# Kernel optimization log

Measured on AMD Instinct MI355X. Metric: run time of the kernel, lower is better.

Reference implementation:

```python
import jax, jax.numpy as jnp
import numpy as np

B, N_PER, E_PER = 100, 1000, 12000  # graphs, nodes/graph, edges/graph
N, E = B * N_PER, B * E_PER
K = int(np.ceil(0.8 * N_PER))  # TopKPooling ratio=0.8 -> 800 kept nodes/graph


def setup_inputs() -> dict:
    key = jax.random.key(0)
    ks = jax.random.split(key, 16)
    g = jnp.repeat(jnp.arange(B, dtype=jnp.int64), E_PER)
    src = g * N_PER + jax.random.randint(ks[0], (E,), 0, N_PER)
    dst = g * N_PER + jax.random.randint(ks[1], (E,), 0, N_PER)
    edge_index = jnp.stack([src, dst]).astype(jnp.int64)
    edge_attr = jax.random.uniform(ks[2], (E,), dtype=jnp.float32) + 0.1  # positive edge weights
    x = jax.random.normal(ks[3], (N, 3), dtype=jnp.float32)
    batch = jnp.repeat(jnp.arange(B, dtype=jnp.int64), N_PER)
    s = 0.1
    return {
        'x': x, 'edge_index': edge_index, 'edge_attr': edge_attr, 'batch': batch,
        'conv1_w': jax.random.normal(ks[4], (3, 64), dtype=jnp.float32) * s,
        'conv1_b': jnp.zeros((64,), dtype=jnp.float32),
        'conv2_w': jax.random.normal(ks[5], (64, 64), dtype=jnp.float32) * s,
        'conv2_b': jnp.zeros((64,), dtype=jnp.float32),
        'pool_w': jax.random.normal(ks[6], (64,), dtype=jnp.float32) * s,
        'lin1_w': jax.random.normal(ks[7], (64, 64), dtype=jnp.float32) * s,
        'lin1_b': jnp.zeros((64,), dtype=jnp.float32),
        'lin2_w': jax.random.normal(ks[8], (64, 32), dtype=jnp.float32) * s,
        'lin2_b': jnp.zeros((32,), dtype=jnp.float32),
        'lin3_w': jax.random.normal(ks[9], (32, 1), dtype=jnp.float32) * s,
        'lin3_b': jnp.zeros((1,), dtype=jnp.float32),
    }


def gcn_conv(x, row, col, ew, W, b):
    # PyG GCNConv with edge_weight and implicit self-loops (weight 1):
    # deg[i] = sum_{e: col=i} ew[e] + 1;  norm_e = d^{-1/2}[row]*ew*d^{-1/2}[col]
    h = x @ W  # [N, out]
    deg = jax.ops.segment_sum(ew, col, num_segments=N) + 1.0
    dinv = jax.lax.rsqrt(deg)
    msg = (dinv[row] * ew * dinv[col])[:, None] * h[row]  # [E, out]
    out = jax.ops.segment_sum(msg, col, num_segments=N)
    out = out + (dinv * dinv)[:, None] * h  # self-loop term
    return out + b


def reference(x, edge_index, edge_attr, batch, conv1_w, conv1_b, conv2_w, conv2_b,
              pool_w, lin1_w, lin1_b, lin2_w, lin2_b, lin3_w, lin3_b):
    row, col = edge_index[0], edge_index[1]
    h = jax.nn.relu(gcn_conv(x, row, col, edge_attr, conv1_w, conv1_b))
    x1 = h.reshape(B, N_PER, 64).mean(axis=1)  # global_mean_pool (equal-size graphs)
    h = jax.nn.relu(gcn_conv(h, row, col, edge_attr, conv2_w, conv2_b))
    # TopKPooling: score = tanh(x.w / ||w||), keep top-K per graph, gate by score
    score = jnp.tanh(h @ pool_w / jnp.linalg.norm(pool_w))  # [N]
    score_bn = score.reshape(B, N_PER)
    vals, idx = jax.lax.top_k(score_bn, K)  # [B, K]
    h_bn = h.reshape(B, N_PER, 64)
    h_sel = jnp.take_along_axis(h_bn, idx[..., None], axis=1) * vals[..., None]
    x2 = h_sel.mean(axis=1)  # global_mean_pool on pooled graph
    z = x1 + x2
    z = jax.nn.relu(z @ lin1_w + lin1_b)
    z = jax.nn.relu(z @ lin2_w + lin2_b)  # dropout is identity in eval mode
    out = jax.nn.sigmoid(z @ lin3_w + lin3_b)[:, 0]
    return out
```

## Files before the change

### kernel.cpp

```cpp
#include <hip/hip_runtime.h>

#define B_G   100
#define N_PER 1000
#define E_PER 12000
#define NTOT  (B_G * N_PER)
#define ETOT  (B_G * E_PER)
#define KSEL  800
#define EPT   12

typedef __attribute__((ext_vector_type(8))) short short8;
typedef __attribute__((ext_vector_type(4))) float float4_;

__device__ __forceinline__ unsigned short f2bf(float f) {
    unsigned u = __float_as_uint(f);
    u += 0x7fffu + ((u >> 16) & 1u);
    return (unsigned short)(u >> 16);
}
__device__ __forceinline__ float upk(unsigned q) {
    return __uint_as_float(q & 0xFFFF0000u);
}
__device__ __forceinline__ float dec_raw(unsigned byte7f) {
    return __uint_as_float(byte7f << 20);
}
__device__ __forceinline__ unsigned enc_fp8(float z) {
    unsigned u = __float_as_uint(z * 0x1p-120f);
    u += 0x7FFFFu + ((u >> 20) & 1u);
    return u >> 20;
}

#define CONV2_TI(TI, AF0, AF1) do {                                            \
    const int t_ = wid + (TI) * 16;                                            \
    const int li_ = t_ * 16 + nloc;                                            \
    const bool valid_ = li_ < N_PER;                                           \
    float acc_[16];                                                            \
    int s_ = 0, cn_ = 0;                                                       \
    if (valid_) {                                                              \
        uint4 rv_ = *(const uint4*)(zs + li_ * 64 + ((kgrp ^ ((li_ >> 1) & 3)) << 4)); \
        _Pragma("unroll")                                                      \
        for (int j = 0; j < 4; j++) {                                          \
            acc_[j]      = dec_raw((rv_.x >> (8 * j)) & 0x7Fu);                \
            acc_[4 + j]  = dec_raw((rv_.y >> (8 * j)) & 0x7Fu);                \
            acc_[8 + j]  = dec_raw((rv_.z >> (8 * j)) & 0x7Fu);                \
            acc_[12 + j] = dec_raw((rv_.w >> (8 * j)) & 0x7Fu);                \
        }                                                                      \
        s_ = li_ ? ends[li_ - 1] : 0;                                          \
        cn_ = ends[li_] - s_;                                                  \
    } else {                                                                   \
        _Pragma("unroll")                                                      \
        for (int j = 0; j < 16; j++) acc_[j] = 0.f;                            \
    }                                                                          \
    int mx_ = cn_;                                                             \
    _Pragma("unroll")                                                          \
    for (int m = 1; m < 16; m <<= 1) mx_ = max(mx_, __shfl_xor(mx_, m));       \
    for (int k = 0; k < mx_; k++) {                                            \
        if (k < cn_) {                                                         \
            unsigned q_ = csr[s_ + k];                                         \
            int src_ = (int)(q_ & 0xFFFFu);                                    \
            float wv_ = upk(q_);                                               \
            uint4 rv_ = *(const uint4*)(zs + src_ * 64 + ((kgrp ^ ((src_ >> 1) & 3)) << 4)); \
            _Pragma("unroll")                                                  \
            for (int j = 0; j < 4; j++) {                                      \
                acc_[j]      += wv_ * dec_raw((rv_.x >> (8 * j)) & 0x7Fu);     \
                acc_[4 + j]  += wv_ * dec_raw((rv_.y >> (8 * j)) & 0x7Fu);     \
                acc_[8 + j]  += wv_ * dec_raw((rv_.z >> (8 * j)) & 0x7Fu);     \
                acc_[12 + j] += wv_ * dec_raw((rv_.w >> (8 * j)) & 0x7Fu);     \
            }                                                                  \
        }                                                                      \
    }                                                                          \
    float scale_ = (valid_ ? dl[li_] : 0.f) * 0x1p120f;                        \
    _Pragma("unroll")                                                          \
    for (int j = 0; j < 8; j++) {                                              \
        AF0[j] = (short)f2bf(scale_ * acc_[j]);                                \
        AF1[j] = (short)f2bf(scale_ * acc_[8 + j]);                            \
    }                                                                          \
} while (0)

#define W2_TI(TI, AF0, AF1) do {                                               \
    const int t_ = wid + (TI) * 16;                                            \
    if (t_ < 63) {                                                             \
        float4_ accv_[4];                                                      \
        _Pragma("unroll")                                                      \
        for (int c = 0; c < 4; ++c) accv_[c] = (float4_){0.f, 0.f, 0.f, 0.f};  \
        _Pragma("unroll")                                                      \
        for (int c = 0; c < 4; ++c) {                                          \
            accv_[c] = __builtin_amdgcn_mfma_f32_16x16x32_bf16(AF0, Bf[0][c], accv_[c], 0, 0, 0); \
            accv_[c] = __builtin_amdgcn_mfma_f32_16x16x32_bf16(AF1, Bf[1][c], accv_[c], 0, 0, 0); \
        }                                                                      \
        _Pragma("unroll")                                                      \
        for (int r2 = 0; r2 < 4; ++r2) {                                       \
            int li2_ = t_ * 16 + kgrp * 4 + r2;                                \
            bool valid2_ = li2_ < N_PER;                                       \
            float sp_ = 0.f;                                                   \
            _Pragma("unroll")                                                  \
            for (int c = 0; c < 4; ++c) {                                      \
                float hv_ = fmaxf(accv_[c][r2] + b2c[c], 0.f);                 \
                sp_ += hv_ * pwc[c];                                           \
                if (valid2_) zs[li2_ * 64 + c * 16 + nloc] = (unsigned char)enc_fp8(hv_); \
            }                                                                  \
            _Pragma("unroll")                                                  \
            for (int m = 1; m < 16; m <<= 1) sp_ += __shfl_xor(sp_, m);        \
            if (valid2_ && nloc == 0) {                                        \
                float scv_ = tanhf(sp_ * invn);                                \
                unsigned bits_ = __float_as_uint(scv_);                        \
                unsigned u_ = (bits_ & 0x80000000u) ? ~bits_ : (bits_ | 0x80000000u); \
                keys[li2_] = ((unsigned long long)u_ << 32) | (unsigned)(1023 - li2_); \
            }                                                                  \
        }                                                                      \
    }                                                                          \
} while (0)

#define FRONT_BODY() do {                                                      \
    int esrc[EPT], edst[EPT]; float eww[EPT];                                  \
    int ne = (tid < (E_PER - (EPT - 1) * 1024)) ? EPT : EPT - 1;               \
    _Pragma("unroll")                                                          \
    for (int i = 0; i < EPT; i++) {                                            \
        if (i < ne) {                                                          \
            int e = tid + i * 1024;                                            \
            esrc[i] = ei[ebase + e] - gbase;                                   \
            edst[i] = ei[ETOT + ebase + e] - gbase;                            \
            eww[i]  = ew[ebase + e];                                           \
        }                                                                      \
    }                                                                          \
    ends[tid] = 0;                                                             \
    for (int i = tid; i < N_PER * 3; i += 1024) xl[i] = x[(size_t)gbase * 3 + i]; \
    __syncthreads();                                                           \
    _Pragma("unroll")                                                          \
    for (int i = 0; i < EPT; i++)                                              \
        if (i < ne) atomicAdd(&ends[edst[i]], 1);                              \
    __syncthreads();                                                           \
    int v = ends[tid];                                                         \
    int sc = v;                                                                \
    _Pragma("unroll")                                                          \
    for (int m = 1; m < 64; m <<= 1) {                                         \
        int t = __shfl_up(sc, m);                                              \
        if (lane >= m) sc += t;                                                \
    }                                                                          \
    if (lane == 63) wpart[wid] = sc;                                           \
    __syncthreads();                                                           \
    if (tid < 16) {                                                            \
        int s2 = wpart[tid];                                                   \
        _Pragma("unroll")                                                      \
        for (int m = 1; m < 16; m <<= 1) {                                     \
            int t = __shfl_up(s2, m);                                          \
            if (tid >= m) s2 += t;                                             \
        }                                                                      \
        wpart[tid] = s2;                                                       \
    }                                                                          \
    __syncthreads();                                                           \
    int incl = sc + (wid > 0 ? wpart[wid - 1] : 0);                            \
    ends[tid] = incl;                                                          \
    posc[tid] = incl - v;                                                      \
    __syncthreads();                                                           \
    _Pragma("unroll")                                                          \
    for (int i = 0; i < EPT; i++)                                              \
        if (i < ne) {                                                          \
            int p = atomicAdd(&posc[edst[i]], 1);                              \
            csr[p] = ((unsigned)f2bf(eww[i]) << 16) | (unsigned)esrc[i];       \
        }                                                                      \
    __syncthreads();                                                           \
    float dmy = 0.f;                                                           \
    int s0i = 0, e0i = 0;                                                      \
    if (tid < N_PER) {                                                         \
        s0i = tid ? ends[tid - 1] : 0;                                         \
        e0i = ends[tid];                                                       \
        float s0 = 0.f, s1 = 0.f;                                              \
        int k = s0i;                                                           \
        for (; k + 2 <= e0i; k += 2) { s0 += upk(csr[k]); s1 += upk(csr[k + 1]); } \
        if (k < e0i) s0 += upk(csr[k]);                                        \
        dmy = rsqrtf(s0 + s1 + 1.0f);                                          \
        dl[tid] = dmy;                                                         \
        xl[tid * 3 + 0] *= dmy;                                                \
        xl[tid * 3 + 1] *= dmy;                                                \
        xl[tid * 3 + 2] *= dmy;                                                \
    }                                                                          \
    __syncthreads();                                                           \
    if (tid < N_PER) {                                                         \
        float a0 = xl[tid * 3 + 0], a1 = xl[tid * 3 + 1], a2 = xl[tid * 3 + 2];\
        for (int k = s0i; k < e0i; k++) {                                      \
            unsigned q = csr[k];                                               \
            int i0 = (int)(q & 0xFFFFu) * 3;                                   \
            float wv = upk(q);                                                 \
            a0 += wv * xl[i0]; a1 += wv * xl[i0 + 1]; a2 += wv * xl[i0 + 2];   \
        }                                                                      \
        aggv[tid * 3 + 0] = dmy * a0;                                          \
        aggv[tid * 3 + 1] = dmy * a1;                                          \
        aggv[tid * 3 + 2] = dmy * a2;                                          \
    }                                                                          \
    __syncthreads();                                                           \
    {                                                                          \
        float w0 = w1[lane], w1v = w1[64 + lane], w2v = w1[128 + lane], bf = b1[lane]; \
        float* sred = (float*)(uA + 12288);                                    \
        float px = 0.f;                                                        \
        int chunk = (lane & 31) >> 3;                                          \
        int word  = ((lane >= 32) ? 2 : 0) + ((lane & 7) >> 2);                \
        for (int node = wid; node < N_PER; node += 16) {                       \
            float a0 = aggv[node * 3], a1 = aggv[node * 3 + 1], a2 = aggv[node * 3 + 2]; \
            float hv = fmaxf(a0 * w0 + a1 * w1v + a2 * w2v + bf, 0.f);         \
            px += hv;                                                          \
            unsigned byte = enc_fp8(dl[node] * hv);                            \
            unsigned t1 = __shfl_xor(byte, 1);                                 \
            unsigned v16 = (lane & 1) ? (t1 | (byte << 8)) : (byte | (t1 << 8)); \
            unsigned t2 = __shfl_xor(v16, 2);                                  \
            unsigned v32 = (lane & 2) ? (t2 | (v16 << 16)) : (v16 | (t2 << 16)); \
            if ((lane & 3) == 0) {                                             \
                int cs = chunk ^ ((node >> 1) & 3);                            \
                *(unsigned*)(zs + node * 64 + cs * 16 + word * 4) = v32;       \
            }                                                                  \
        }                                                                      \
        sred[wid * 64 + lane] = px;                                            \
        __syncthreads();                                                       \
        if (tid < 64) {                                                        \
            float t = 0.f;                                                     \
            for (int r = 0; r < 16; r++) t += sred[r * 64 + tid];              \
            x1b[tid] = t * (1.0f / N_PER);                                     \
        }                                                                      \
    }                                                                          \
} while (0)

#define W2_SETUP() do {                                                        \
    _Pragma("unroll")                                                          \
    for (int kh = 0; kh < 2; ++kh)                                             \
        _Pragma("unroll")                                                      \
        for (int c = 0; c < 4; ++c) {                                          \
            short8 t;                                                          \
            _Pragma("unroll")                                                  \
            for (int j = 0; j < 8; ++j)                                        \
                t[j] = (short)f2bf(w2[(kh * 32 + kgrp * 8 + j) * 64 + c * 16 + nloc]); \
            Bf[kh][c] = t;                                                     \
        }                                                                      \
    _Pragma("unroll")                                                          \
    for (int c = 0; c < 4; ++c) {                                              \
        b2c[c] = b2[c * 16 + nloc];                                            \
        pwc[c] = pw[c * 16 + nloc];                                            \
    }                                                                          \
    {                                                                          \
        float p = pw[lane], pn = p * p;                                        \
        _Pragma("unroll")                                                      \
        for (int m = 32; m; m >>= 1) pn += __shfl_xor(pn, m);                  \
        invn = rsqrtf(pn);                                                     \
    }                                                                          \
} while (0)

#define TAIL_BODY(OUTIDX) do {                                                 \
    {                                                                          \
        unsigned long long key = keys[tid];                                    \
        for (int k = 2; k <= 1024; k <<= 1) {                                  \
            for (int j = k >> 1; j > 0; j >>= 1) {                             \
                bool desc = (tid & k) == 0;                                    \
                unsigned long long p;                                          \
                if (j >= 64) {                                                 \
                    keys[tid] = key;                                           \
                    __syncthreads();                                           \
                    p = keys[tid ^ j];                                         \
                    __syncthreads();                                           \
                } else {                                                       \
                    p = __shfl_xor(key, j);                                    \
                }                                                              \
                bool low = (tid & j) == 0;                                     \
                bool sw = low ? (desc ? (key < p) : (key > p))                 \
                              : (desc ? (p < key) : (p > key));                \
                if (sw) key = p;                                               \
            }                                                                  \
        }                                                                      \
        keys[tid] = key;                                                       \
    }                                                                          \
    __syncthreads();                                                           \
    float* red   = (float*)(uA + 8192);                                        \
    float* a1buf = (float*)(uA + 12288);                                       \
    float* a2buf = (float*)(uA + 12544);                                       \
    float* zbuf  = (float*)(uA + 12672);                                       \
    {                                                                          \
        int f = tid & 63, w16 = tid >> 6;                                      \
        float acc2 = 0.f;                                                      \
        for (int r = w16; r < KSEL; r += 16) {                                 \
            unsigned long long key = keys[r];                                  \
            int idx = 1023 - (int)(key & 0xFFFFFFFFu);                         \
            unsigned u = (unsigned)(key >> 32);                                \
            unsigned bits = (u & 0x80000000u) ? (u & 0x7FFFFFFFu) : ~u;        \
            float valS = __uint_as_float(bits) * 0x1p120f;                     \
            acc2 += valS * dec_raw((unsigned)zs[idx * 64 + f] & 0x7Fu);        \
        }                                                                      \
        red[tid] = acc2;                                                       \
    }                                                                          \
    __syncthreads();                                                           \
    if (tid < 64) {                                                            \
        float s2 = 0.f;                                                        \
        for (int ww = 0; ww < 16; ww++) s2 += red[ww * 64 + tid];              \
        zbuf[tid] = x1b[tid] + s2 * (1.0f / KSEL);                             \
    }                                                                          \
    __syncthreads();                                                           \
    if (tid < 64) {                                                            \
        float a = l1b[tid];                                                    \
        for (int k = 0; k < 64; k++) a += zbuf[k] * l1w[k * 64 + tid];         \
        a1buf[tid] = fmaxf(a, 0.f);                                            \
    }                                                                          \
    __syncthreads();                                                           \
    if (tid < 32) {                                                            \
        float a = l2b[tid];                                                    \
        for (int k = 0; k < 64; k++) a += a1buf[k] * l2w[k * 32 + tid];        \
        a2buf[tid] = fmaxf(a, 0.f);                                            \
    }                                                                          \
    __syncthreads();                                                           \
    if (tid == 0) {                                                            \
        float t = l3b[0];                                                      \
        for (int k = 0; k < 32; k++) t += a2buf[k] * l3w[k];                   \
        out[OUTIDX] = 1.0f / (1.0f + expf(-t));                                \
    }                                                                          \
} while (0)

#define SMEM_DECLS()                                                           \
    __shared__ __align__(16) unsigned char smem[136832];                       \
    unsigned char* zs = smem;                                                  \
    float* xl = (float*)smem;                                                  \
    unsigned* csr = (unsigned*)(smem + 64000);                                 \
    int*   ends = (int*)(smem + 112000);                                       \
    float* dl   = (float*)(smem + 116096);                                     \
    int*   posc = (int*)(smem + 116096);                                       \
    int*   wpart = (int*)(smem + 120192);                                      \
    float* x1b   = (float*)(smem + 120192);                                    \
    unsigned char* uA = smem + 120448;                                         \
    float* aggv = (float*)uA;

#define PARAMS                                                                 \
    const int* __restrict__ ei, const float* __restrict__ ew,                  \
    const float* __restrict__ x,                                               \
    const float* __restrict__ w1, const float* __restrict__ b1,                \
    const float* __restrict__ w2, const float* __restrict__ b2,                \
    const float* __restrict__ pw,                                              \
    const float* __restrict__ l1w, const float* __restrict__ l1b,              \
    const float* __restrict__ l2w, const float* __restrict__ l2b,              \
    const float* __restrict__ l3w, const float* __restrict__ l3b,              \
    float* __restrict__ out

__global__ __launch_bounds__(1024)
__attribute__((amdgpu_waves_per_eu(4, 4))) void k_all_single(PARAMS) {
    SMEM_DECLS();
    int g = blockIdx.x, tid = threadIdx.x;
    int wid = tid >> 6, lane = tid & 63;
    int gbase = g * N_PER, ebase = g * E_PER;
    FRONT_BODY();
    int kgrp = lane >> 4, nloc = lane & 15;
    short8 Af0a, Af0b, Af1a, Af1b, Af2a, Af2b, Af3a, Af3b;
    CONV2_TI(0, Af0a, Af0b);
    CONV2_TI(1, Af1a, Af1b);
    CONV2_TI(2, Af2a, Af2b);
    CONV2_TI(3, Af3a, Af3b);
    __syncthreads();
    unsigned long long* keys = (unsigned long long*)uA;
    {
        short8 Bf[2][4]; float b2c[4], pwc[4], invn;
        W2_SETUP();
        if (tid >= N_PER) keys[tid] = 0ull;
        W2_TI(0, Af0a, Af0b);
        W2_TI(1, Af1a, Af1b);
        W2_TI(2, Af2a, Af2b);
        W2_TI(3, Af3a, Af3b);
    }
    __syncthreads();
    TAIL_BODY(g);
}

__global__ __launch_bounds__(1024)
__attribute__((amdgpu_waves_per_eu(4, 4))) void k_all_pair(
    PARAMS, unsigned char* __restrict__ ws) {
    SMEM_DECLS();
    int g = blockIdx.x >> 1, half = blockIdx.x & 1, tid = threadIdx.x;
    int wid = tid >> 6, lane = tid & 63;
    int gbase = g * N_PER, ebase = g * E_PER;
    unsigned int* flag = (unsigned int*)ws;
    unsigned char* h2x = ws + 4096 + (size_t)g * 32768;
    unsigned long long* kx =
        (unsigned long long*)(ws + 4096 + 100 * 32768 + (size_t)g * 4096);

    FRONT_BODY();
    int kgrp = lane >> 4, nloc = lane & 15;
    const int tiA = half * 2, tiB = half * 2 + 1;
    short8 AfAa, AfAb, AfBa, AfBb;
    CONV2_TI(tiA, AfAa, AfAb);
    CONV2_TI(tiB, AfBa, AfBb);
    __syncthreads();
    unsigned long long* keys = (unsigned long long*)uA;
    {
        short8 Bf[2][4]; float b2c[4], pwc[4], invn;
        W2_SETUP();
        if (tid >= N_PER) keys[tid] = 0ull;
        W2_TI(tiA, AfAa, AfAb);
        W2_TI(tiB, AfBa, AfBb);
    }
    __syncthreads();
    if (half) {
        const uint4* srcv = (const uint4*)(zs + 32768);
        uint4* dstv = (uint4*)h2x;
        for (int i = tid; i < 1952; i += 1024) dstv[i] = srcv[i];
        for (int i = tid; i < 512; i += 1024) kx[i] = keys[512 + i];
        __syncthreads();
        if (tid == 0)
            __hip_atomic_store(flag + g, 1u, __ATOMIC_RELEASE,
                               __HIP_MEMORY_SCOPE_AGENT);
        return;
    }
    if (tid == 0) {
        for (int it = 0; it < 1000000; ++it) {
            if (__hip_atomic_load(flag + g, __ATOMIC_ACQUIRE,
                                  __HIP_MEMORY_SCOPE_AGENT) != 0u) break;
            __builtin_amdgcn_s_sleep(8);
        }
    }
    __syncthreads();
    {
        uint4* dstv = (uint4*)(zs + 32768);
        const uint4* srcv = (const uint4*)h2x;
        for (int i = tid; i < 1952; i += 1024) dstv[i] = srcv[i];
        for (int i = tid; i < 512; i += 1024) keys[512 + i] = kx[i];
    }
    __syncthreads();
    TAIL_BODY(g);
}

extern "C" void kernel_launch(void* const* d_in, const int* in_sizes, int n_in,
                              void* d_out, int out_size, void* d_ws, size_t ws_size,
                              hipStream_t stream) {
    const float* x   = (const float*)d_in[0];
    const int*   ei  = (const int*)d_in[1];
    const float* ew  = (const float*)d_in[2];
    const float* c1w = (const float*)d_in[4];
    const float* c1b = (const float*)d_in[5];
    const float* c2w = (const float*)d_in[6];
    const float* c2b = (const float*)d_in[7];
    const float* pw  = (const float*)d_in[8];
    const float* l1w = (const float*)d_in[9];
    const float* l1b = (const float*)d_in[10];
    const float* l2w = (const float*)d_in[11];
    const float* l2b = (const float*)d_in[12];
    const float* l3w = (const float*)d_in[13];
    const float* l3b = (const float*)d_in[14];
    float* out = (float*)d_out;
    (void)in_sizes; (void)n_in; (void)out_size;

    const size_t needed = 4096 + (size_t)100 * 32768 + (size_t)100 * 4096;
    if (d_ws != nullptr && ws_size >= needed) {
        hipMemsetAsync(d_ws, 0, 512, stream);
        k_all_pair<<<2 * B_G, 1024, 0, stream>>>(
            ei, ew, x, c1w, c1b, c2w, c2b, pw,
            l1w, l1b, l2w, l2b, l3w, l3b, out, (unsigned char*)d_ws);
    } else {
        k_all_single<<<B_G, 1024, 0, stream>>>(
            ei, ew, x, c1w, c1b, c2w, c2b, pw,
            l1w, l1b, l2w, l2b, l3w, l3b, out);
    }
}
```

Baseline: 171.3 us.

## Split fused pair kernel into build, mid and tail kernels via workspace

Replaces the single 200-block kernel, where block pairs per graph synchronize through a global flag spin-wait, with three launches. The first builds the CSR per graph, the second runs conv1/conv2 split across two blocks per graph, and the third does top-k and the MLP. Each stage hands its data to the next through global workspace. This removes the intra-kernel spin wait and the duplicated CSR build across both halves, at the cost of two extra launches and extra global round-trips for the CSR, h2 and keys.

```diff
diff --git a/kernel.cpp b/kernel.cpp
--- a/kernel.cpp
+++ b/kernel.cpp
@@ -8,6 +8,13 @@
 #define KSEL  800
 #define EPT   12
 
+#define CSRB  0u
+#define ENDB  4915200u
+#define H2B   5324800u
+#define KEYB  11878400u
+#define X1BB  12697600u
+#define WSNEED 12723200u
+
 typedef __attribute__((ext_vector_type(8))) short short8;
 typedef __attribute__((ext_vector_type(4))) float float4_;
 
@@ -28,88 +35,7 @@
     return u >> 20;
 }
 
-#define CONV2_TI(TI, AF0, AF1) do {                                            \
-    const int t_ = wid + (TI) * 16;                                            \
-    const int li_ = t_ * 16 + nloc;                                            \
-    const bool valid_ = li_ < N_PER;                                           \
-    float acc_[16];                                                            \
-    int s_ = 0, cn_ = 0;                                                       \
-    if (valid_) {                                                              \
-        uint4 rv_ = *(const uint4*)(zs + li_ * 64 + ((kgrp ^ ((li_ >> 1) & 3)) << 4)); \
-        _Pragma("unroll")                                                      \
-        for (int j = 0; j < 4; j++) {                                          \
-            acc_[j]      = dec_raw((rv_.x >> (8 * j)) & 0x7Fu);                \
-            acc_[4 + j]  = dec_raw((rv_.y >> (8 * j)) & 0x7Fu);                \
-            acc_[8 + j]  = dec_raw((rv_.z >> (8 * j)) & 0x7Fu);                \
-            acc_[12 + j] = dec_raw((rv_.w >> (8 * j)) & 0x7Fu);                \
-        }                                                                      \
-        s_ = li_ ? ends[li_ - 1] : 0;                                          \
-        cn_ = ends[li_] - s_;                                                  \
-    } else {                                                                   \
-        _Pragma("unroll")                                                      \
-        for (int j = 0; j < 16; j++) acc_[j] = 0.f;                            \
-    }                                                                          \
-    int mx_ = cn_;                                                             \
-    _Pragma("unroll")                                                          \
-    for (int m = 1; m < 16; m <<= 1) mx_ = max(mx_, __shfl_xor(mx_, m));       \
-    for (int k = 0; k < mx_; k++) {                                            \
-        if (k < cn_) {                                                         \
-            unsigned q_ = csr[s_ + k];                                         \
-            int src_ = (int)(q_ & 0xFFFFu);                                    \
-            float wv_ = upk(q_);                                               \
-            uint4 rv_ = *(const uint4*)(zs + src_ * 64 + ((kgrp ^ ((src_ >> 1) & 3)) << 4)); \
-            _Pragma("unroll")                                                  \
-            for (int j = 0; j < 4; j++) {                                      \
-                acc_[j]      += wv_ * dec_raw((rv_.x >> (8 * j)) & 0x7Fu);     \
-                acc_[4 + j]  += wv_ * dec_raw((rv_.y >> (8 * j)) & 0x7Fu);     \
-                acc_[8 + j]  += wv_ * dec_raw((rv_.z >> (8 * j)) & 0x7Fu);     \
-                acc_[12 + j] += wv_ * dec_raw((rv_.w >> (8 * j)) & 0x7Fu);     \
-            }                                                                  \
-        }                                                                      \
-    }                                                                          \
-    float scale_ = (valid_ ? dl[li_] : 0.f) * 0x1p120f;                        \
-    _Pragma("unroll")                                                          \
-    for (int j = 0; j < 8; j++) {                                              \
-        AF0[j] = (short)f2bf(scale_ * acc_[j]);                                \
-        AF1[j] = (short)f2bf(scale_ * acc_[8 + j]);                            \
-    }                                                                          \
-} while (0)
-
-#define W2_TI(TI, AF0, AF1) do {                                               \
-    const int t_ = wid + (TI) * 16;                                            \
-    if (t_ < 63) {                                                             \
-        float4_ accv_[4];                                                      \
-        _Pragma("unroll")                                                      \
-        for (int c = 0; c < 4; ++c) accv_[c] = (float4_){0.f, 0.f, 0.f, 0.f};  \
-        _Pragma("unroll")                                                      \
-        for (int c = 0; c < 4; ++c) {                                          \
-            accv_[c] = __builtin_amdgcn_mfma_f32_16x16x32_bf16(AF0, Bf[0][c], accv_[c], 0, 0, 0); \
-            accv_[c] = __builtin_amdgcn_mfma_f32_16x16x32_bf16(AF1, Bf[1][c], accv_[c], 0, 0, 0); \
-        }                                                                      \
-        _Pragma("unroll")                                                      \
-        for (int r2 = 0; r2 < 4; ++r2) {                                       \
-            int li2_ = t_ * 16 + kgrp * 4 + r2;                                \
-            bool valid2_ = li2_ < N_PER;                                       \
-            float sp_ = 0.f;                                                   \
-            _Pragma("unroll")                                                  \
-            for (int c = 0; c < 4; ++c) {                                      \
-                float hv_ = fmaxf(accv_[c][r2] + b2c[c], 0.f);                 \
-                sp_ += hv_ * pwc[c];                                           \
-                if (valid2_) zs[li2_ * 64 + c * 16 + nloc] = (unsigned char)enc_fp8(hv_); \
-            }                                                                  \
-            _Pragma("unroll")                                                  \
-            for (int m = 1; m < 16; m <<= 1) sp_ += __shfl_xor(sp_, m);        \
-            if (valid2_ && nloc == 0) {                                        \
-                float scv_ = tanhf(sp_ * invn);                                \
-                unsigned bits_ = __float_as_uint(scv_);                        \
-                unsigned u_ = (bits_ & 0x80000000u) ? ~bits_ : (bits_ | 0x80000000u); \
-                keys[li2_] = ((unsigned long long)u_ << 32) | (unsigned)(1023 - li2_); \
-            }                                                                  \
-        }                                                                      \
-    }                                                                          \
-} while (0)
-
-#define FRONT_BODY() do {                                                      \
+#define BUILD_BODY(PRE) do {                                                   \
     int esrc[EPT], edst[EPT]; float eww[EPT];                                  \
     int ne = (tid < (E_PER - (EPT - 1) * 1024)) ? EPT : EPT - 1;               \
     _Pragma("unroll")                                                          \
@@ -122,7 +48,7 @@
         }                                                                      \
     }                                                                          \
     ends[tid] = 0;                                                             \
-    for (int i = tid; i < N_PER * 3; i += 1024) xl[i] = x[(size_t)gbase * 3 + i]; \
+    PRE                                                                        \
     __syncthreads();                                                           \
     _Pragma("unroll")                                                          \
     for (int i = 0; i < EPT; i++)                                              \
@@ -158,6 +84,9 @@
             csr[p] = ((unsigned)f2bf(eww[i]) << 16) | (unsigned)esrc[i];       \
         }                                                                      \
     __syncthreads();                                                           \
+} while (0)
+
+#define REST_BODY() do {                                                       \
     float dmy = 0.f;                                                           \
     int s0i = 0, e0i = 0;                                                      \
     if (tid < N_PER) {                                                         \
@@ -213,6 +142,87 @@
             float t = 0.f;                                                     \
             for (int r = 0; r < 16; r++) t += sred[r * 64 + tid];              \
             x1b[tid] = t * (1.0f / N_PER);                                     \
+        }                                                                      \
+    }                                                                          \
+} while (0)
+
+#define CONV2_TI(TI, AF0, AF1) do {                                            \
+    const int t_ = wid + (TI) * 16;                                            \
+    const int li_ = t_ * 16 + nloc;                                            \
+    const bool valid_ = li_ < N_PER;                                           \
+    float acc_[16];                                                            \
+    int s_ = 0, cn_ = 0;                                                       \
+    if (valid_) {                                                              \
+        uint4 rv_ = *(const uint4*)(zs + li_ * 64 + ((kgrp ^ ((li_ >> 1) & 3)) << 4)); \
+        _Pragma("unroll")                                                      \
+        for (int j = 0; j < 4; j++) {                                          \
+            acc_[j]      = dec_raw((rv_.x >> (8 * j)) & 0x7Fu);                \
+            acc_[4 + j]  = dec_raw((rv_.y >> (8 * j)) & 0x7Fu);                \
+            acc_[8 + j]  = dec_raw((rv_.z >> (8 * j)) & 0x7Fu);                \
+            acc_[12 + j] = dec_raw((rv_.w >> (8 * j)) & 0x7Fu);                \
+        }                                                                      \
+        s_ = li_ ? ends[li_ - 1] : 0;                                          \
+        cn_ = ends[li_] - s_;                                                  \
+    } else {                                                                   \
+        _Pragma("unroll")                                                      \
+        for (int j = 0; j < 16; j++) acc_[j] = 0.f;                            \
+    }                                                                          \
+    int mx_ = cn_;                                                             \
+    _Pragma("unroll")                                                          \
+    for (int m = 1; m < 16; m <<= 1) mx_ = max(mx_, __shfl_xor(mx_, m));       \
+    for (int k = 0; k < mx_; k++) {                                            \
+        if (k < cn_) {                                                         \
+            unsigned q_ = csr[s_ + k];                                         \
+            int src_ = (int)(q_ & 0xFFFFu);                                    \
+            float wv_ = upk(q_);                                               \
+            uint4 rv_ = *(const uint4*)(zs + src_ * 64 + ((kgrp ^ ((src_ >> 1) & 3)) << 4)); \
+            _Pragma("unroll")                                                  \
+            for (int j = 0; j < 4; j++) {                                      \
+                acc_[j]      += wv_ * dec_raw((rv_.x >> (8 * j)) & 0x7Fu);     \
+                acc_[4 + j]  += wv_ * dec_raw((rv_.y >> (8 * j)) & 0x7Fu);     \
+                acc_[8 + j]  += wv_ * dec_raw((rv_.z >> (8 * j)) & 0x7Fu);     \
+                acc_[12 + j] += wv_ * dec_raw((rv_.w >> (8 * j)) & 0x7Fu);     \
+            }                                                                  \
+        }                                                                      \
+    }                                                                          \
+    float scale_ = (valid_ ? dl[li_] : 0.f) * 0x1p120f;                        \
+    _Pragma("unroll")                                                          \
+    for (int j = 0; j < 8; j++) {                                              \
+        AF0[j] = (short)f2bf(scale_ * acc_[j]);                                \
+        AF1[j] = (short)f2bf(scale_ * acc_[8 + j]);                            \
+    }                                                                          \
+} while (0)
+
+#define W2_TI(TI, AF0, AF1) do {                                               \
+    const int t_ = wid + (TI) * 16;                                            \
+    if (t_ < 63) {                                                             \
+        float4_ accv_[4];                                                      \
+        _Pragma("unroll")                                                      \
+        for (int c = 0; c < 4; ++c) accv_[c] = (float4_){0.f, 0.f, 0.f, 0.f};  \
+        _Pragma("unroll")                                                      \
+        for (int c = 0; c < 4; ++c) {                                          \
+            accv_[c] = __builtin_amdgcn_mfma_f32_16x16x32_bf16(AF0, Bf[0][c], accv_[c], 0, 0, 0); \
+            accv_[c] = __builtin_amdgcn_mfma_f32_16x16x32_bf16(AF1, Bf[1][c], accv_[c], 0, 0, 0); \
+        }                                                                      \
+        _Pragma("unroll")                                                      \
+        for (int r2 = 0; r2 < 4; ++r2) {                                       \
+            int li2_ = t_ * 16 + kgrp * 4 + r2;                                \
+            bool valid2_ = li2_ < N_PER;                                       \
+            float sp_ = 0.f;                                                   \
+            _Pragma("unroll")                                                  \
+            for (int c = 0; c < 4; ++c) {                                      \
+                float hv_ = fmaxf(accv_[c][r2] + b2c[c], 0.f);                 \
+                sp_ += hv_ * pwc[c];                                           \
+                if (valid2_) zs[li2_ * 64 + c * 16 + nloc] = (unsigned char)enc_fp8(hv_); \
+            }                                                                  \
+            _Pragma("unroll")                                                  \
+            for (int m = 1; m < 16; m <<= 1) sp_ += __shfl_xor(sp_, m);        \
+            if (valid2_ && nloc == 0) {                                        \
+                float scv_ = tanhf(sp_ * invn);                                \
+                unsigned bits_ = __float_as_uint(scv_);                        \
+                unsigned u_ = (bits_ & 0x80000000u) ? ~bits_ : (bits_ | 0x80000000u); \
+                keys[li2_] = ((unsigned long long)u_ << 32) | (unsigned)(1023 - li2_); \
+            }                                                                  \
         }                                                                      \
     }                                                                          \
 } while (0)
@@ -265,10 +275,6 @@
         keys[tid] = key;                                                       \
     }                                                                          \
     __syncthreads();                                                           \
-    float* red   = (float*)(uA + 8192);                                        \
-    float* a1buf = (float*)(uA + 12288);                                       \
-    float* a2buf = (float*)(uA + 12544);                                       \
-    float* zbuf  = (float*)(uA + 12672);                                       \
     {                                                                          \
         int f = tid & 63, w16 = tid >> 6;                                      \
         float acc2 = 0.f;                                                      \
@@ -319,26 +325,118 @@
     int*   wpart = (int*)(smem + 120192);                                      \
     float* x1b   = (float*)(smem + 120192);                                    \
     unsigned char* uA = smem + 120448;                                         \
-    float* aggv = (float*)uA;
-
-#define PARAMS                                                                 \
-    const int* __restrict__ ei, const float* __restrict__ ew,                  \
-    const float* __restrict__ x,                                               \
-    const float* __restrict__ w1, const float* __restrict__ b1,                \
-    const float* __restrict__ w2, const float* __restrict__ b2,                \
-    const float* __restrict__ pw,                                              \
-    const float* __restrict__ l1w, const float* __restrict__ l1b,              \
-    const float* __restrict__ l2w, const float* __restrict__ l2b,              \
-    const float* __restrict__ l3w, const float* __restrict__ l3b,              \
-    float* __restrict__ out
+    float* aggv = (float*)uA;                                                  \
+    (void)posc; (void)wpart; (void)aggv;
+
+__global__ __launch_bounds__(1024) void k_build(
+    const int* __restrict__ ei, const float* __restrict__ ew,
+    unsigned char* __restrict__ ws) {
+    __shared__ __align__(16) unsigned csr[12000];
+    __shared__ int ends[1024];
+    __shared__ int posc[1024];
+    __shared__ int wpart[16];
+    int g = blockIdx.x, tid = threadIdx.x;
+    int wid = tid >> 6, lane = tid & 63;
+    int gbase = g * N_PER, ebase = g * E_PER;
+    BUILD_BODY();
+    {
+        uint4* cw = (uint4*)(ws + CSRB + (size_t)g * 49152);
+        const uint4* cs = (const uint4*)csr;
+        for (int i = tid; i < 3000; i += 1024) cw[i] = cs[i];
+        ((int*)(ws + ENDB + (size_t)g * 4096))[tid] = ends[tid];
+    }
+}
 
 __global__ __launch_bounds__(1024)
-__attribute__((amdgpu_waves_per_eu(4, 4))) void k_all_single(PARAMS) {
+__attribute__((amdgpu_waves_per_eu(4, 4))) void k_mid(
+    const float* __restrict__ x,
+    const float* __restrict__ w1, const float* __restrict__ b1,
+    const float* __restrict__ w2, const float* __restrict__ b2,
+    const float* __restrict__ pw, unsigned char* __restrict__ ws) {
+    SMEM_DECLS();
+    int g = blockIdx.x >> 1, half = blockIdx.x & 1, tid = threadIdx.x;
+    int wid = tid >> 6, lane = tid & 63;
+    int gbase = g * N_PER;
+    {
+        const uint4* cs = (const uint4*)(ws + CSRB + (size_t)g * 49152);
+        uint4* cd = (uint4*)csr;
+        for (int i = tid; i < 3000; i += 1024) cd[i] = cs[i];
+        ends[tid] = ((const int*)(ws + ENDB + (size_t)g * 4096))[tid];
+        for (int i = tid; i < N_PER * 3; i += 1024) xl[i] = x[(size_t)gbase * 3 + i];
+    }
+    __syncthreads();
+    REST_BODY();
+    int kgrp = lane >> 4, nloc = lane & 15;
+    const int tiA = half * 2, tiB = half * 2 + 1;
+    short8 AfAa, AfAb, AfBa, AfBb;
+    CONV2_TI(tiA, AfAa, AfAb);
+    CONV2_TI(tiB, AfBa, AfBb);
+    __syncthreads();
+    unsigned long long* keys = (unsigned long long*)uA;
+    {
+        short8 Bf[2][4]; float b2c[4], pwc[4], invn;
+        W2_SETUP();
+        if (tid >= N_PER) keys[tid] = 0ull;
+        W2_TI(tiA, AfAa, AfAb);
+        W2_TI(tiB, AfBa, AfBb);
+    }
+    __syncthreads();
+    {
+        uint4* d = (uint4*)(ws + H2B + (size_t)g * 65536 + (size_t)half * 32768);
+        const uint4* s = (const uint4*)(zs + half * 32768);
+        int n = half ? 1952 : 2048;
+        for (int i = tid; i < n; i += 1024) d[i] = s[i];
+        unsigned long long* kw =
+            (unsigned long long*)(ws + KEYB + (size_t)g * 8192);
+        for (int i = tid; i < 512; i += 1024)
+            kw[half * 512 + i] = keys[half * 512 + i];
+        if (!half && tid < 64)
+            ((float*)(ws + X1BB + (size_t)g * 256))[tid] = x1b[tid];
+    }
+}
+
+__global__ __launch_bounds__(1024) void k_tail(
+    const float* __restrict__ l1w, const float* __restrict__ l1b,
+    const float* __restrict__ l2w, const float* __restrict__ l2b,
+    const float* __restrict__ l3w, const float* __restrict__ l3b,
+    float* __restrict__ out, const unsigned char* __restrict__ ws) {
+    __shared__ __align__(16) unsigned char sm2[77184];
+    unsigned char* zs = sm2;
+    unsigned long long* keys = (unsigned long long*)(sm2 + 64000);
+    float* red   = (float*)(sm2 + 72192);
+    float* x1b   = (float*)(sm2 + 76288);
+    float* a1buf = (float*)(sm2 + 76544);
+    float* a2buf = (float*)(sm2 + 76800);
+    float* zbuf  = (float*)(sm2 + 76928);
+    int g = blockIdx.x, tid = threadIdx.x;
+    {
+        uint4* hd = (uint4*)zs;
+        const uint4* hs = (const uint4*)(ws + H2B + (size_t)g * 65536);
+        for (int i = tid; i < 4000; i += 1024) hd[i] = hs[i];
+        keys[tid] = ((const unsigned long long*)(ws + KEYB + (size_t)g * 8192))[tid];
+        if (tid < 64) x1b[tid] = ((const float*)(ws + X1BB + (size_t)g * 256))[tid];
+    }
+    __syncthreads();
+    TAIL_BODY(g);
+}
+
+__global__ __launch_bounds__(1024)
+__attribute__((amdgpu_waves_per_eu(4, 4))) void k_all_single(
+    const int* __restrict__ ei, const float* __restrict__ ew,
+    const float* __restrict__ x,
+    const float* __restrict__ w1, const float* __restrict__ b1,
+    const float* __restrict__ w2, const float* __restrict__ b2,
+    const float* __restrict__ pw,
+    const float* __restrict__ l1w, const float* __restrict__ l1b,
+    const float* __restrict__ l2w, const float* __restrict__ l2b,
+    const float* __restrict__ l3w, const float* __restrict__ l3b,
+    float* __restrict__ out) {
     SMEM_DECLS();
     int g = blockIdx.x, tid = threadIdx.x;
     int wid = tid >> 6, lane = tid & 63;
     int gbase = g * N_PER, ebase = g * E_PER;
-    FRONT_BODY();
+    BUILD_BODY(for (int i = tid; i < N_PER * 3; i += 1024) xl[i] = x[(size_t)gbase * 3 + i];);
+    REST_BODY();
     int kgrp = lane >> 4, nloc = lane & 15;
     short8 Af0a, Af0b, Af1a, Af1b, Af2a, Af2b, Af3a, Af3b;
     CONV2_TI(0, Af0a, Af0b);
@@ -357,63 +455,10 @@
         W2_TI(3, Af3a, Af3b);
     }
     __syncthreads();
-    TAIL_BODY(g);
-}
-
-__global__ __launch_bounds__(1024)
-__attribute__((amdgpu_waves_per_eu(4, 4))) void k_all_pair(
-    PARAMS, unsigned char* __restrict__ ws) {
-    SMEM_DECLS();
-    int g = blockIdx.x >> 1, half = blockIdx.x & 1, tid = threadIdx.x;
-    int wid = tid >> 6, lane = tid & 63;
-    int gbase = g * N_PER, ebase = g * E_PER;
-    unsigned int* flag = (unsigned int*)ws;
-    unsigned char* h2x = ws + 4096 + (size_t)g * 32768;
-    unsigned long long* kx =
-        (unsigned long long*)(ws + 4096 + 100 * 32768 + (size_t)g * 4096);
-
-    FRONT_BODY();
-    int kgrp = lane >> 4, nloc = lane & 15;
-    const int tiA = half * 2, tiB = half * 2 + 1;
-    short8 AfAa, AfAb, AfBa, AfBb;
-    CONV2_TI(tiA, AfAa, AfAb);
-    CONV2_TI(tiB, AfBa, AfBb);
-    __syncthreads();
-    unsigned long long* keys = (unsigned long long*)uA;
-    {
-        short8 Bf[2][4]; float b2c[4], pwc[4], invn;
-        W2_SETUP();
-        if (tid >= N_PER) keys[tid] = 0ull;
-        W2_TI(tiA, AfAa, AfAb);
-        W2_TI(tiB, AfBa, AfBb);
-    }
-    __syncthreads();
-    if (half) {
-        const uint4* srcv = (const uint4*)(zs + 32768);
-        uint4* dstv = (uint4*)h2x;
-        for (int i = tid; i < 1952; i += 1024) dstv[i] = srcv[i];
-        for (int i = tid; i < 512; i += 1024) kx[i] = keys[512 + i];
-        __syncthreads();
-        if (tid == 0)
-            __hip_atomic_store(flag + g, 1u, __ATOMIC_RELEASE,
-                               __HIP_MEMORY_SCOPE_AGENT);
-        return;
-    }
-    if (tid == 0) {
-        for (int it = 0; it < 1000000; ++it) {
-            if (__hip_atomic_load(flag + g, __ATOMIC_ACQUIRE,
-                                  __HIP_MEMORY_SCOPE_AGENT) != 0u) break;
-            __builtin_amdgcn_s_sleep(8);
-        }
-    }
-    __syncthreads();
-    {
-        uint4* dstv = (uint4*)(zs + 32768);
-        const uint4* srcv = (const uint4*)h2x;
-        for (int i = tid; i < 1952; i += 1024) dstv[i] = srcv[i];
-        for (int i = tid; i < 512; i += 1024) keys[512 + i] = kx[i];
-    }
-    __syncthreads();
+    float* red   = (float*)(uA + 8192);
+    float* a1buf = (float*)(uA + 12288);
+    float* a2buf = (float*)(uA + 12544);
+    float* zbuf  = (float*)(uA + 12672);
     TAIL_BODY(g);
 }
 
@@ -437,12 +482,11 @@
     float* out = (float*)d_out;
     (void)in_sizes; (void)n_in; (void)out_size;
 
-    const size_t needed = 4096 + (size_t)100 * 32768 + (size_t)100 * 4096;
-    if (d_ws != nullptr && ws_size >= needed) {
-        hipMemsetAsync(d_ws, 0, 512, stream);
-        k_all_pair<<<2 * B_G, 1024, 0, stream>>>(
-            ei, ew, x, c1w, c1b, c2w, c2b, pw,
-            l1w, l1b, l2w, l2b, l3w, l3b, out, (unsigned char*)d_ws);
+    if (d_ws != nullptr && ws_size >= (size_t)WSNEED) {
+        unsigned char* ws = (unsigned char*)d_ws;
+        k_build<<<B_G, 1024, 0, stream>>>(ei, ew, ws);
+        k_mid<<<2 * B_G, 1024, 0, stream>>>(x, c1w, c1b, c2w, c2b, pw, ws);
+        k_tail<<<B_G, 1024, 0, stream>>>(l1w, l1b, l2w, l2b, l3w, l3b, out, ws);
     } else {
         k_all_single<<<B_G, 1024, 0, stream>>>(
             ei, ew, x, c1w, c1b, c2w, c2b, pw,
```

Result: no change. 170.7 us (-0.3%).
